# Performance work log

Hardware: AMD Instinct MI355X
Metric: run time of the kernel (lower is better)

## Reference

```python
import jax, jax.numpy as jnp
import numpy as np

N = 100000      # number of vertices
E = 3200000     # number of directed edges (avg degree 32)
EPS = 1e-8
WEIGHT = 0.01


def setup_inputs() -> dict:
    key = jax.random.key(0)
    k1, k2, k3, k4 = jax.random.split(key, 4)
    mu0 = jax.random.normal(k1, (N, 3), dtype=jnp.float32)
    # current positions = canonical + small deformation (realistic ARAP setting)
    mu = mu0 + 0.1 * jax.random.normal(k2, (N, 3), dtype=jnp.float32)
    i = jax.random.randint(k3, (E,), 0, N, dtype=jnp.int32)
    # avoid self-edges (rest length 0 would give w = 1/eps = 1e8 and swamp the loss)
    off = jax.random.randint(k4, (E,), 1, N, dtype=jnp.int32)
    j = (i + off) % N
    edge_idx = jnp.stack([i, j], axis=0)  # (2, E)
    return {"mu0": mu0, "mu": mu, "edge_idx": edge_idx}


def reference(mu0, mu, edge_idx):
    i, j = edge_idx[0], edge_idx[1]
    rest = mu0[j] - mu0[i]        # (E,3) canonical edge vectors
    deform = mu[j] - mu[i]        # (E,3) deformed edge vectors
    w = 1.0 / (jnp.linalg.norm(rest, axis=-1) + EPS)  # (E,)
    # per-edge weighted outer product deform \otimes rest
    outer = jnp.einsum('e,ei,ej->eij', w, deform, rest)  # (E,3,3)
    # scatter-add into per-node covariance matrices
    S = jnp.zeros((mu0.shape[0], 3, 3), dtype=mu0.dtype).at[i].add(outer)  # (N,3,3)
    U, _, Vh = jnp.linalg.svd(S, full_matrices=False)
    R = U @ Vh
    det_mask = (jnp.linalg.det(R) < 0)[:, None, None]
    diag_fix = jnp.array([-1.0, 1.0, 1.0], dtype=mu0.dtype).reshape(1, 1, 3)
    Vh = jnp.where(det_mask, Vh * diag_fix, Vh)
    R = U @ Vh                      # (N,3,3) best-fit rotations
    Ri = R[i]                       # (E,3,3)
    pred = jnp.einsum('eij,ej->ei', Ri, rest)
    err = deform - pred
    loss = jnp.sum(w * jnp.sum(err * err, axis=-1)) / jnp.sum(w)
    return WEIGHT * loss
```

## Files before the change

### kernel.cpp

```cpp
#include <hip/hip_runtime.h>
#include <hip/hip_fp16.h>
#include <math.h>

#define EPS     1e-8f
#define MP      128
#define MP_BITS 7
#define JBITS   17
#define JMASK   ((1u << JBITS) - 1u)
#define CAP     6144
#define PMAX    1024
#define MAXPT   12
#define NCHUNK  12800
#define EPT     25

struct alignas(16) Pk { __half2 a, b, c; unsigned pad; };

__global__ __launch_bounds__(256) void k_pack(
    const float* __restrict__ mu0, const float* __restrict__ mu,
    Pk* __restrict__ pk, int N)
{
    int n = blockIdx.x * blockDim.x + threadIdx.x;
    if (n >= N) return;
    float x0 = mu0[3*n+0], y0 = mu0[3*n+1], z0 = mu0[3*n+2];
    float x1 = mu [3*n+0], y1 = mu [3*n+1], z1 = mu [3*n+2];
    Pk o;
    o.a = __floats2half2_rn(x0, y0);
    o.b = __floats2half2_rn(z0, x1);
    o.c = __floats2half2_rn(y1, z1);
    o.pad = 0u;
    pk[n] = o;
}

__global__ __launch_bounds__(256) void k_init(int* __restrict__ gcursor, int P)
{
    int t = blockIdx.x * blockDim.x + threadIdx.x;
    if (t < P) gcursor[t] = t * CAP;
}

__global__ __launch_bounds__(512) void k_bin(
    const int* __restrict__ ei, const int* __restrict__ ej,
    int* __restrict__ gcursor, unsigned* __restrict__ bucket,
    int E, int P)
{
    __shared__ int cnt[PMAX];
    __shared__ int base[PMAX];
    int lo = blockIdx.x * NCHUNK;
    int hi = lo + NCHUNK; if (hi > E) hi = E;

    for (int t = threadIdx.x; t < P; t += 512) cnt[t] = 0;

    int myi[EPT];
    #pragma unroll
    for (int k = 0; k < EPT; ++k) {
        int e = lo + threadIdx.x + k * 512;
        myi[k] = (e < hi) ? ei[e] : -1;
    }
    __syncthreads();

    #pragma unroll
    for (int k = 0; k < EPT; ++k)
        if (myi[k] >= 0) atomicAdd(&cnt[myi[k] >> MP_BITS], 1);
    __syncthreads();

    for (int t = threadIdx.x; t < P; t += 512) {
        int c = cnt[t];
        base[t] = c ? atomicAdd(&gcursor[t], c) : 0;
        cnt[t] = 0;
    }
    __syncthreads();

    #pragma unroll
    for (int k = 0; k < EPT; ++k) {
        int e = lo + threadIdx.x + k * 512;
        if (e < hi) {
            int i = myi[k];
            int j = ej[e];
            int p = i >> MP_BITS;
            int off = atomicAdd(&cnt[p], 1);
            int pos = base[p] + off;
            if (pos < (p + 1) * CAP)
                bucket[pos] = ((unsigned)(i & (MP - 1)) << JBITS) | (unsigned)j;
        }
    }
}

__global__ __launch_bounds__(512) void k_accum(
    const float* __restrict__ mu0, const float* __restrict__ mu,
    const Pk* __restrict__ pk,
    const unsigned* __restrict__ bucket, const int* __restrict__ gcursor,
    double* __restrict__ pblk, int N)
{
    __shared__ unsigned sorted[CAP];
    __shared__ int hist[MP];
    __shared__ int offs[MP];
    __shared__ int cursor[MP];
    __shared__ int sc[MP];
    __shared__ float Sl[MP * 9];
    __shared__ double redw[8], rede[8];

    int p = blockIdx.x;
    int lo_n = p << MP_BITS;
    int beg = p * CAP;
    int end = gcursor[p];
    int cap_end = beg + CAP;
    if (end > cap_end) end = cap_end;

    for (int t = threadIdx.x; t < MP; t += 512) hist[t] = 0;
    __syncthreads();

    unsigned myu[MAXPT];
    int mycnt = 0;
    {
        int e = beg + threadIdx.x;
        #pragma unroll
        for (int k = 0; k < MAXPT; ++k) {
            if (e < end) {
                unsigned uu = bucket[e];
                myu[k] = uu;
                atomicAdd(&hist[uu >> JBITS], 1);
                ++mycnt;
            }
            e += 512;
        }
    }
    __syncthreads();

    if (threadIdx.x < MP) {
        int v = hist[threadIdx.x];
        int incl = v;
        #pragma unroll
        for (int d = 1; d < 64; d <<= 1) {
            int o = __shfl_up(incl, d);
            if ((threadIdx.x & 63) >= d) incl += o;
        }
        sc[threadIdx.x] = incl;
    }
    __syncthreads();
    if (threadIdx.x < MP) {
        int carry = (threadIdx.x >= 64) ? sc[63] : 0;
        int excl = sc[threadIdx.x] - hist[threadIdx.x] + carry;
        offs[threadIdx.x] = excl;
        cursor[threadIdx.x] = excl;
    }
    __syncthreads();

    #pragma unroll
    for (int k = 0; k < MAXPT; ++k) {
        if (k < mycnt) {
            unsigned uu = myu[k];
            int li = (int)(uu >> JBITS);
            int pos = atomicAdd(&cursor[li], 1);
            sorted[pos] = uu;
        }
    }
    __syncthreads();

    double wsum = 0.0, errsum = 0.0;
    float S[9] = {0.f,0.f,0.f,0.f,0.f,0.f,0.f,0.f,0.f};
    {
        int node = threadIdx.x >> 2;
        int part = threadIdx.x & 3;
        int n = lo_n + node;
        if (node < MP && n < N) {
            float ax = mu0[3*n+0], ay = mu0[3*n+1], az = mu0[3*n+2];
            float cx = mu [3*n+0], cy = mu [3*n+1], cz = mu [3*n+2];

            auto body = [&](const Pk& cc) {
                float2 f01 = __half22float2(cc.a);
                float2 f23 = __half22float2(cc.b);
                float2 f45 = __half22float2(cc.c);
                float r0 = f01.x - ax, r1 = f01.y - ay, r2 = f23.x - az;
                float d0 = f23.y - cx, d1 = f45.x - cy, d2 = f45.y - cz;
                float rr = r0*r0 + r1*r1 + r2*r2;
                float dd = d0*d0 + d1*d1 + d2*d2;
                float w  = 1.0f / (sqrtf(rr) + EPS);
                wsum   += (double)w;
                errsum += (double)(w * (dd + rr));
                float wd0 = w*d0, wd1 = w*d1, wd2 = w*d2;
                S[0] += wd0*r0; S[1] += wd0*r1; S[2] += wd0*r2;
                S[3] += wd1*r0; S[4] += wd1*r1; S[5] += wd1*r2;
                S[6] += wd2*r0; S[7] += wd2*r1; S[8] += wd2*r2;
            };

            int b0 = offs[node];
            int e1 = b0 + hist[node];
            int e  = b0 + part;
            for (; e + 4 < e1; e += 8) {
                unsigned u0 = sorted[e], u1 = sorted[e + 4];
                Pk c0 = pk[u0 & JMASK];
                Pk c1 = pk[u1 & JMASK];
                body(c0);
                body(c1);
            }
            if (e < e1) {
                Pk c0 = pk[sorted[e] & JMASK];
                body(c0);
            }
        }
        #pragma unroll
        for (int c = 0; c < 9; ++c) {
            S[c] += __shfl_down(S[c], 2);
            S[c] += __shfl_down(S[c], 1);
        }
        if (part == 0 && node < MP)
            #pragma unroll
            for (int c = 0; c < 9; ++c) Sl[node*9 + c] = S[c];
    }
    __syncthreads();

    if (threadIdx.x < MP && lo_n + (int)threadIdx.x < N) {
        float Sf[9], X[9];
        #pragma unroll
        for (int c = 0; c < 9; ++c) { Sf[c] = Sl[threadIdx.x*9 + c]; X[c] = Sf[c]; }
        bool ok = true;
        #pragma unroll
        for (int it = 0; it < 8; ++it) {
            float c00 =  (X[4]*X[8] - X[5]*X[7]);
            float c01 = -(X[3]*X[8] - X[5]*X[6]);
            float c02 =  (X[3]*X[7] - X[4]*X[6]);
            float c10 = -(X[1]*X[8] - X[2]*X[7]);
            float c11 =  (X[0]*X[8] - X[2]*X[6]);
            float c12 = -(X[0]*X[7] - X[1]*X[6]);
            float c20 =  (X[1]*X[5] - X[2]*X[4]);
            float c21 = -(X[0]*X[5] - X[2]*X[3]);
            float c22 =  (X[0]*X[4] - X[1]*X[3]);
            float det = X[0]*c00 + X[1]*c01 + X[2]*c02;
            if (!(fabsf(det) > 1e-30f)) { ok = false; break; }
            float inv_det = 1.0f / det;
            float Y[9] = { c00*inv_det, c01*inv_det, c02*inv_det,
                           c10*inv_det, c11*inv_det, c12*inv_det,
                           c20*inv_det, c21*inv_det, c22*inv_det };
            float nx = 0.f, ny = 0.f;
            #pragma unroll
            for (int c = 0; c < 9; ++c) { nx += X[c]*X[c]; ny += Y[c]*Y[c]; }
            float g = sqrtf(sqrtf(ny / nx));
            float hg = 0.5f * g, hig = 0.5f / g;
            #pragma unroll
            for (int c = 0; c < 9; ++c) X[c] = hg * X[c] + hig * Y[c];
        }
        if (!ok) {
            X[0]=1.f; X[1]=0.f; X[2]=0.f;
            X[3]=0.f; X[4]=1.f; X[5]=0.f;
            X[6]=0.f; X[7]=0.f; X[8]=1.f;
        }
        float det = X[0]*(X[4]*X[8] - X[5]*X[7])
                  - X[1]*(X[3]*X[8] - X[5]*X[6])
                  + X[2]*(X[3]*X[7] - X[4]*X[6]);
        if (det < 0.f) { X[0] = -X[0]; X[3] = -X[3]; X[6] = -X[6]; }
        float tr = X[0]*Sf[0] + X[1]*Sf[1] + X[2]*Sf[2]
                 + X[3]*Sf[3] + X[4]*Sf[4] + X[5]*Sf[5]
                 + X[6]*Sf[6] + X[7]*Sf[7] + X[8]*Sf[8];
        errsum -= 2.0 * (double)tr;
    }

    #pragma unroll
    for (int off = 32; off > 0; off >>= 1) {
        wsum   += __shfl_down(wsum, off);
        errsum += __shfl_down(errsum, off);
    }
    if ((threadIdx.x & 63) == 0) {
        redw[threadIdx.x >> 6] = wsum;
        rede[threadIdx.x >> 6] = errsum;
    }
    __syncthreads();
    if (threadIdx.x == 0) {
        double W = 0.0, Er = 0.0;
        #pragma unroll
        for (int k = 0; k < 8; ++k) { W += redw[k]; Er += rede[k]; }
        pblk[2*p]   = W;
        pblk[2*p+1] = Er;
    }
}

__global__ __launch_bounds__(256) void k_final(
    const double* __restrict__ pblk, int nb, float* __restrict__ out)
{
    __shared__ double sw[4], se[4];
    double w = 0.0, e = 0.0;
    for (int t = threadIdx.x; t < nb; t += 256) {
        w += pblk[2*t];
        e += pblk[2*t+1];
    }
    #pragma unroll
    for (int off = 32; off > 0; off >>= 1) {
        w += __shfl_down(w, off);
        e += __shfl_down(e, off);
    }
    if ((threadIdx.x & 63) == 0) {
        sw[threadIdx.x >> 6] = w;
        se[threadIdx.x >> 6] = e;
    }
    __syncthreads();
    if (threadIdx.x == 0) {
        double W  = sw[0] + sw[1] + sw[2] + sw[3];
        double Er = se[0] + se[1] + se[2] + se[3];
        out[0] = (float)(0.01 * (Er / W));
    }
}

extern "C" void kernel_launch(void* const* d_in, const int* in_sizes, int n_in,
                              void* d_out, int out_size, void* d_ws, size_t ws_size,
                              hipStream_t stream) {
    const float* mu0 = (const float*)d_in[0];
    const float* mu  = (const float*)d_in[1];
    const int*   eidx = (const int*)d_in[2];
    int N = in_sizes[0] / 3;
    int E = in_sizes[2] / 2;
    const int* ei = eidx;
    const int* ej = eidx + E;

    int P = (N + MP - 1) / MP;

    double*   pblk    = (double*)d_ws;
    int*      gcursor = (int*)((char*)d_ws + 2 * PMAX * sizeof(double));
    Pk*       pk      = (Pk*)((char*)d_ws + 2 * PMAX * sizeof(double) + PMAX * sizeof(int));
    unsigned* bucket  = (unsigned*)(pk + N);

    int nbin = (E + NCHUNK - 1) / NCHUNK;

    k_pack  <<<(N + 255) / 256, 256, 0, stream>>>(mu0, mu, pk, N);
    k_init  <<<(P + 255) / 256, 256, 0, stream>>>(gcursor, P);
    k_bin   <<<nbin, 512, 0, stream>>>(ei, ej, gcursor, bucket, E, P);
    k_accum <<<P, 512, 0, stream>>>(mu0, mu, pk, bucket, gcursor, pblk, N);
    k_final <<<1, 256, 0, stream>>>(pblk, P, (float*)d_out);
}
```

Before: 140.4 us.

## Rebalance binning partitions, fuse init into pack, use nontemporal loads

Partitions become 131 nodes each, so there are about 764 partitions instead of 782, fewer than 256 CUs times 3. The accumulate kernel now runs 576 threads per block (131×4 nodes), with the scan extended to three wavefronts. The binning kernel runs exactly 256 blocks, sized from E, so the work maps to the CUs evenly. The cursor init kernel is merged into the pack kernel. Bucket and edge traffic uses nontemporal loads and stores, and the own-node coordinates are read from the packed half buffer. The risks are division by a non-power-of-two, half-precision own coordinates changing numerics, and the larger block size.

```diff
diff --git a/kernel.cpp b/kernel.cpp
--- a/kernel.cpp
+++ b/kernel.cpp
@@ -3,23 +3,24 @@
 #include <math.h>
 
 #define EPS     1e-8f
-#define MP      128
-#define MP_BITS 7
+#define MP      131
 #define JBITS   17
 #define JMASK   ((1u << JBITS) - 1u)
 #define CAP     6144
 #define PMAX    1024
-#define MAXPT   12
-#define NCHUNK  12800
+#define ACC_T   576
+#define MAXPT   11
+#define BIN_T   512
 #define EPT     25
 
 struct alignas(16) Pk { __half2 a, b, c; unsigned pad; };
 
-__global__ __launch_bounds__(256) void k_pack(
+__global__ __launch_bounds__(256) void k_prep(
     const float* __restrict__ mu0, const float* __restrict__ mu,
-    Pk* __restrict__ pk, int N)
+    Pk* __restrict__ pk, int* __restrict__ gcursor, int N, int P)
 {
     int n = blockIdx.x * blockDim.x + threadIdx.x;
+    if (n < P) gcursor[n] = n * CAP;
     if (n >= N) return;
     float x0 = mu0[3*n+0], y0 = mu0[3*n+1], z0 = mu0[3*n+2];
     float x1 = mu [3*n+0], y1 = mu [3*n+1], z1 = mu [3*n+2];
@@ -31,38 +32,32 @@
     pk[n] = o;
 }
 
-__global__ __launch_bounds__(256) void k_init(int* __restrict__ gcursor, int P)
-{
-    int t = blockIdx.x * blockDim.x + threadIdx.x;
-    if (t < P) gcursor[t] = t * CAP;
-}
-
-__global__ __launch_bounds__(512) void k_bin(
+__global__ __launch_bounds__(BIN_T) void k_bin(
     const int* __restrict__ ei, const int* __restrict__ ej,
     int* __restrict__ gcursor, unsigned* __restrict__ bucket,
-    int E, int P)
+    int E, int P, int nchunk)
 {
     __shared__ int cnt[PMAX];
     __shared__ int base[PMAX];
-    int lo = blockIdx.x * NCHUNK;
-    int hi = lo + NCHUNK; if (hi > E) hi = E;
-
-    for (int t = threadIdx.x; t < P; t += 512) cnt[t] = 0;
+    int lo = blockIdx.x * nchunk;
+    int hi = lo + nchunk; if (hi > E) hi = E;
+
+    for (int t = threadIdx.x; t < P; t += BIN_T) cnt[t] = 0;
 
     int myi[EPT];
     #pragma unroll
     for (int k = 0; k < EPT; ++k) {
-        int e = lo + threadIdx.x + k * 512;
-        myi[k] = (e < hi) ? ei[e] : -1;
+        int e = lo + threadIdx.x + k * BIN_T;
+        myi[k] = (e < hi) ? __builtin_nontemporal_load(&ei[e]) : -1;
     }
     __syncthreads();
 
     #pragma unroll
     for (int k = 0; k < EPT; ++k)
-        if (myi[k] >= 0) atomicAdd(&cnt[myi[k] >> MP_BITS], 1);
-    __syncthreads();
-
-    for (int t = threadIdx.x; t < P; t += 512) {
+        if (myi[k] >= 0) atomicAdd(&cnt[(unsigned)myi[k] / (unsigned)MP], 1);
+    __syncthreads();
+
+    for (int t = threadIdx.x; t < P; t += BIN_T) {
         int c = cnt[t];
         base[t] = c ? atomicAdd(&gcursor[t], c) : 0;
         cnt[t] = 0;
@@ -71,21 +66,22 @@
 
     #pragma unroll
     for (int k = 0; k < EPT; ++k) {
-        int e = lo + threadIdx.x + k * 512;
+        int e = lo + threadIdx.x + k * BIN_T;
         if (e < hi) {
             int i = myi[k];
-            int j = ej[e];
-            int p = i >> MP_BITS;
+            int j = __builtin_nontemporal_load(&ej[e]);
+            int p = (int)((unsigned)i / (unsigned)MP);
+            int li = i - p * MP;
             int off = atomicAdd(&cnt[p], 1);
             int pos = base[p] + off;
             if (pos < (p + 1) * CAP)
-                bucket[pos] = ((unsigned)(i & (MP - 1)) << JBITS) | (unsigned)j;
-        }
-    }
-}
-
-__global__ __launch_bounds__(512) void k_accum(
-    const float* __restrict__ mu0, const float* __restrict__ mu,
+                __builtin_nontemporal_store(
+                    ((unsigned)li << JBITS) | (unsigned)j, &bucket[pos]);
+        }
+    }
+}
+
+__global__ __launch_bounds__(ACC_T) void k_accum(
     const Pk* __restrict__ pk,
     const unsigned* __restrict__ bucket, const int* __restrict__ gcursor,
     double* __restrict__ pblk, int N)
@@ -94,18 +90,18 @@
     __shared__ int hist[MP];
     __shared__ int offs[MP];
     __shared__ int cursor[MP];
-    __shared__ int sc[MP];
+    __shared__ int sc[192];
     __shared__ float Sl[MP * 9];
-    __shared__ double redw[8], rede[8];
+    __shared__ double redw[9], rede[9];
 
     int p = blockIdx.x;
-    int lo_n = p << MP_BITS;
+    int lo_n = p * MP;
     int beg = p * CAP;
     int end = gcursor[p];
     int cap_end = beg + CAP;
     if (end > cap_end) end = cap_end;
 
-    for (int t = threadIdx.x; t < MP; t += 512) hist[t] = 0;
+    for (int t = threadIdx.x; t < MP; t += ACC_T) hist[t] = 0;
     __syncthreads();
 
     unsigned myu[MAXPT];
@@ -115,18 +111,18 @@
         #pragma unroll
         for (int k = 0; k < MAXPT; ++k) {
             if (e < end) {
-                unsigned uu = bucket[e];
+                unsigned uu = __builtin_nontemporal_load(&bucket[e]);
                 myu[k] = uu;
                 atomicAdd(&hist[uu >> JBITS], 1);
                 ++mycnt;
             }
-            e += 512;
-        }
-    }
-    __syncthreads();
-
-    if (threadIdx.x < MP) {
-        int v = hist[threadIdx.x];
+            e += ACC_T;
+        }
+    }
+    __syncthreads();
+
+    if (threadIdx.x < 192) {
+        int v = (threadIdx.x < MP) ? hist[threadIdx.x] : 0;
         int incl = v;
         #pragma unroll
         for (int d = 1; d < 64; d <<= 1) {
@@ -137,7 +133,10 @@
     }
     __syncthreads();
     if (threadIdx.x < MP) {
-        int carry = (threadIdx.x >= 64) ? sc[63] : 0;
+        int w = threadIdx.x >> 6;
+        int carry = 0;
+        if (w >= 1) carry += sc[63];
+        if (w >= 2) carry += sc[127];
         int excl = sc[threadIdx.x] - hist[threadIdx.x] + carry;
         offs[threadIdx.x] = excl;
         cursor[threadIdx.x] = excl;
@@ -162,8 +161,12 @@
         int part = threadIdx.x & 3;
         int n = lo_n + node;
         if (node < MP && n < N) {
-            float ax = mu0[3*n+0], ay = mu0[3*n+1], az = mu0[3*n+2];
-            float cx = mu [3*n+0], cy = mu [3*n+1], cz = mu [3*n+2];
+            Pk ac = pk[n];
+            float2 a01 = __half22float2(ac.a);
+            float2 a23 = __half22float2(ac.b);
+            float2 a45 = __half22float2(ac.c);
+            float ax = a01.x, ay = a01.y, az = a23.x;
+            float cx = a23.y, cy = a45.x, cz = a45.y;
 
             auto body = [&](const Pk& cc) {
                 float2 f01 = __half22float2(cc.a);
@@ -266,7 +269,7 @@
     if (threadIdx.x == 0) {
         double W = 0.0, Er = 0.0;
         #pragma unroll
-        for (int k = 0; k < 8; ++k) { W += redw[k]; Er += rede[k]; }
+        for (int k = 0; k < 9; ++k) { W += redw[k]; Er += rede[k]; }
         pblk[2*p]   = W;
         pblk[2*p+1] = Er;
     }
@@ -316,11 +319,15 @@
     Pk*       pk      = (Pk*)((char*)d_ws + 2 * PMAX * sizeof(double) + PMAX * sizeof(int));
     unsigned* bucket  = (unsigned*)(pk + N);
 
-    int nbin = (E + NCHUNK - 1) / NCHUNK;
-
-    k_pack  <<<(N + 255) / 256, 256, 0, stream>>>(mu0, mu, pk, N);
-    k_init  <<<(P + 255) / 256, 256, 0, stream>>>(gcursor, P);
-    k_bin   <<<nbin, 512, 0, stream>>>(ei, ej, gcursor, bucket, E, P);
-    k_accum <<<P, 512, 0, stream>>>(mu0, mu, pk, bucket, gcursor, pblk, N);
+    int nbin   = 256;
+    int nchunk = (E + nbin - 1) / nbin;
+    if (nchunk > EPT * BIN_T) {
+        nchunk = EPT * BIN_T;
+        nbin = (E + nchunk - 1) / nchunk;
+    }
+
+    k_prep  <<<(N + 255) / 256, 256, 0, stream>>>(mu0, mu, pk, gcursor, N, P);
+    k_bin   <<<nbin, BIN_T, 0, stream>>>(ei, ej, gcursor, bucket, E, P, nchunk);
+    k_accum <<<P, ACC_T, 0, stream>>>(pk, bucket, gcursor, pblk, N);
     k_final <<<1, 256, 0, stream>>>(pblk, P, (float*)d_out);
 }
```

Result: slower. 208.3 us (+48.3%).
